# Performance work log

Hardware: AMD Instinct MI355X
Metric: run time of the kernel (lower is better)

## Reference

```python
import jax, jax.numpy as jnp
import numpy as np

B, M, N_, H, C, D = 2, 64, 64, 2, 8, 4  # batch, lattice m, lattice n, heads, channels, head_dim


def get_irpe(R):
    # R: (h, m, n) -> P[h, i, j] = R[h, (xi-xj) mod m, (yi-yj) mod n]
    # (negative fancy-index wrap in the original == modular indexing)
    h, m, n = R.shape
    dx = (jnp.arange(m)[:, None] - jnp.arange(m)[None, :]) % m  # (m, m)
    dy = (jnp.arange(n)[:, None] - jnp.arange(n)[None, :]) % n  # (n, n)
    P = R[:, dx[:, None, :, None], dy[None, :, None, :]]  # (h, m, n, m, n)
    return P.reshape(h, m * n, m * n)


def circ_conv(x, W, b, groups=1):
    # NHWC conv with CIRCULAR padding (flax 'CIRCULAR' == wrap-pad then VALID)
    ph, pw = W.shape[0] // 2, W.shape[1] // 2
    if ph or pw:
        x = jnp.pad(x, ((0, 0), (ph, ph), (pw, pw), (0, 0)), mode='wrap')
    y = jax.lax.conv_general_dilated(x, W, (1, 1), 'VALID',
                                     dimension_numbers=('NHWC', 'HWIO', 'NHWC'),
                                     feature_group_count=groups)
    return y + b


def setup_inputs() -> dict:
    key = jax.random.key(0)
    ks = jax.random.split(key, 10)
    m, n, c, h, d = M, N_, C, H, D

    def nrm(k, shape, fan_in):
        return jax.random.normal(k, shape, jnp.float32) * np.float32(np.sqrt(1.0 / fan_in))

    return {
        'x': jax.random.normal(ks[0], (B, m, n, c), jnp.float32),
        'conv_W': nrm(ks[1], (3, 3, c, c), 9 * c / 2),         # he_normal
        'conv_b': jnp.zeros((c,), jnp.float32),
        'Wq': nrm(ks[2], (c, h * d), c),                       # lecun_normal
        'Wk': nrm(ks[3], (c, h * d), c),
        'Wv': nrm(ks[4], (c, h * d), c),
        'pos': nrm(ks[5], (h, m, n), h * m),                   # lecun_normal on (h,m,n)
        'Wo': nrm(ks[6], (h * d, c), h * d),
        'mlp1_W': nrm(ks[7], (1, 1, c, 4 * c), c / 2),         # he_normal
        'mlp1_b': jnp.zeros((4 * c,), jnp.float32),
        'mlp2_W': nrm(ks[8], (3, 3, 1, 4 * c), 9),             # depthwise, lecun
        'mlp2_b': jnp.zeros((4 * c,), jnp.float32),
        'mlp3_W': nrm(ks[9], (1, 1, 4 * c, c), 4 * c / 2),     # he_normal
        'mlp3_b': jnp.zeros((c,), jnp.float32),
    }


def reference(x, conv_W, conv_b, Wq, Wk, Wv, pos, Wo,
              mlp1_W, mlp1_b, mlp2_W, mlp2_b, mlp3_W, mlp3_b):
    b_, m, n, c = x.shape
    h, d = H, D
    # ---- conv block (norm = 1) ----
    res = x
    x = circ_conv(jax.nn.gelu(x / np.float32(1.0)), conv_W, conv_b) + res
    # ---- attention (norm = 2) ----
    res = x
    y = x / np.float32(np.sqrt(2.0))

    def heads(z, W):
        # (b,m,n,c) @ (c,h*d) -> (b,h,N,d), last dim split order (h,d) as in einops
        return jnp.einsum('bmnc,ce->bmne', z, W).reshape(b_, m * n, h, d).transpose(0, 2, 1, 3)

    q, k, v = heads(y, Wq), heads(y, Wk), heads(y, Wv)
    P = get_irpe(pos)[None]  # (1, h, N, N)
    attn = jax.nn.softmax((jnp.einsum('bhnd,bhmd->bhnm', q, k) + P) / np.float32(np.sqrt(d)))
    # faithful to source: 'bhnn,bhnd->bhnd' uses the DIAGONAL of attn to scale v
    a = jnp.einsum('bhnn,bhnd->bhnd', attn, v)
    a = a.transpose(0, 2, 1, 3).reshape(b_, m * n, h * d)  # b n (h d)
    x = (a @ Wo).reshape(b_, m, n, c) + res
    # ---- MLP (norm = 3) ----
    res = x
    y = x / np.float32(np.sqrt(3.0))
    y = jax.nn.gelu(circ_conv(y, mlp1_W, mlp1_b))
    y = jax.nn.gelu(circ_conv(y, mlp2_W, mlp2_b, groups=4 * c))
    return circ_conv(y, mlp3_W, mlp3_b) + res
```

## Files before the change

kernel.cpp:

```cpp
#include <hip/hip_runtime.h>
#include <math.h>

#define Tt 4096
#define KCH 32

#define QSCALE 0.72134752044448170f

__device__ __forceinline__ float gelu_tanh(float x) {
  float x3 = x * x * x;
  float u2 = 2.3022081159f * (x + 0.044715f * x3);
  float e = __builtin_amdgcn_exp2f(u2);
  float th = 1.0f - 2.0f * __builtin_amdgcn_rcpf(e + 1.0f);
  return 0.5f * x * (1.0f + th);
}

__global__ __launch_bounds__(64) void k_pre(
    const float* __restrict__ x, const float* __restrict__ cW,
    const float* __restrict__ cb, const float* __restrict__ Wq,
    const float* __restrict__ Wk, const float* __restrict__ Wv,
    float* __restrict__ x1, float* __restrict__ qo,
    float* __restrict__ ko, float* __restrict__ vo) {
  const int bi = blockIdx.x;
  const int b = bi >> 6, i = bi & 63;
  const int j = threadIdx.x;
  float acc[8];
#pragma unroll
  for (int c = 0; c < 8; c++) acc[c] = cb[c];
#pragma unroll
  for (int di = 0; di < 3; di++) {
    const int ii = (i + di + 63) & 63;
#pragma unroll
    for (int dj = 0; dj < 3; dj++) {
      const int jj = (j + dj + 63) & 63;
      const float4* px = (const float4*)(x + ((b * 64 + ii) * 64 + jj) * 8);
      float4 a0 = px[0], a1 = px[1];
      float g[8];
      g[0] = gelu_tanh(a0.x); g[1] = gelu_tanh(a0.y);
      g[2] = gelu_tanh(a0.z); g[3] = gelu_tanh(a0.w);
      g[4] = gelu_tanh(a1.x); g[5] = gelu_tanh(a1.y);
      g[6] = gelu_tanh(a1.z); g[7] = gelu_tanh(a1.w);
      const float* w = cW + (di * 3 + dj) * 64;
#pragma unroll
      for (int ci = 0; ci < 8; ci++) {
        const float gv = g[ci];
#pragma unroll
        for (int c = 0; c < 8; c++) acc[c] += gv * w[ci * 8 + c];
      }
    }
  }
  const int t = i * 64 + j;
  const float4* pxc = (const float4*)(x + (b * Tt + t) * 8);
  float4 c0 = pxc[0], c1 = pxc[1];
  float xv[8];
  xv[0] = acc[0] + c0.x; xv[1] = acc[1] + c0.y;
  xv[2] = acc[2] + c0.z; xv[3] = acc[3] + c0.w;
  xv[4] = acc[4] + c1.x; xv[5] = acc[5] + c1.y;
  xv[6] = acc[6] + c1.z; xv[7] = acc[7] + c1.w;
  float4* px1 = (float4*)(x1 + (b * Tt + t) * 8);
  px1[0] = make_float4(xv[0], xv[1], xv[2], xv[3]);
  px1[1] = make_float4(xv[4], xv[5], xv[6], xv[7]);
  float y[8];
#pragma unroll
  for (int c = 0; c < 8; c++) y[c] = xv[c] * 0.7071067811865475f;
#pragma unroll
  for (int h = 0; h < 2; h++) {
    float qe[4], ke[4], ve[4];
#pragma unroll
    for (int d = 0; d < 4; d++) {
      const int e = h * 4 + d;
      float sq = 0.f, sk = 0.f, sv = 0.f;
#pragma unroll
      for (int c = 0; c < 8; c++) {
        sq += y[c] * Wq[c * 8 + e];
        sk += y[c] * Wk[c * 8 + e];
        sv += y[c] * Wv[c * 8 + e];
      }
      qe[d] = sq * QSCALE;
      ke[d] = sk; ve[d] = sv;
    }
    const int idx = (b * 2 + h) * Tt + t;
    ((float4*)qo)[idx] = make_float4(qe[0], qe[1], qe[2], qe[3]);
    ((float4*)ko)[idx] = make_float4(ke[0], ke[1], ke[2], ke[3]);
    ((float4*)vo)[idx] = make_float4(ve[0], ve[1], ve[2], ve[3]);
  }
}

__global__ __launch_bounds__(128) void k_attn(
    const float* __restrict__ qo, const float* __restrict__ ko,
    const float* __restrict__ pos, float* __restrict__ part) {
  const int id = blockIdx.x;
  const int qpair = id & 31;
  const int bh = (id >> 5) & 3;
  const int chunk = id >> 7;
  const int h = bh & 1;
  const int wave = threadIdx.x >> 6;
  const int lane = threadIdx.x & 63;
  const int qblk = qpair * 2 + wave;
  __shared__ float posr[2][2][128];
  __shared__ float4 ks[128];
#pragma unroll
  for (int r = 0; r < 2; r++) {
    const int j1 = chunk * 2 + r;
    const int row = (qblk - j1) & 63;
    const float v = QSCALE * pos[(h * 64 + row) * 64 + lane];
    posr[wave][r][lane] = v;
    posr[wave][r][lane + 64] = v;
  }
  const float4* kp = (const float4*)ko + bh * Tt + chunk * 128;
  ks[threadIdx.x] = kp[threadIdx.x];
  __syncthreads();
  const int t1 = qblk * 64 + lane;
  const float4 qv = ((const float4*)qo)[bh * Tt + t1];
  float Z0 = 0.0f, Z1 = 0.0f;
#pragma unroll
  for (int r = 0; r < 2; r++) {
    const float* prow = &posr[wave][r][lane + 1];
    const float4* kr = &ks[r * 64];
#pragma unroll 8
    for (int j2 = 0; j2 < 64; j2 += 2) {
      const float4 ka = kr[j2];
      const float4 kb = kr[j2 + 1];
      const float ba = prow[63 - j2];
      const float bb = prow[62 - j2];
      const float sa = fmaf(qv.x, ka.x, fmaf(qv.y, ka.y,
                       fmaf(qv.z, ka.z, fmaf(qv.w, ka.w, ba))));
      const float sb = fmaf(qv.x, kb.x, fmaf(qv.y, kb.y,
                       fmaf(qv.z, kb.z, fmaf(qv.w, kb.w, bb))));
      Z0 += __builtin_amdgcn_exp2f(sa);
      Z1 += __builtin_amdgcn_exp2f(sb);
    }
  }
  part[(chunk * 4 + bh) * Tt + t1] = Z0 + Z1;
}

__global__ __launch_bounds__(64) void k_post(
    const float* __restrict__ part, const float* __restrict__ qo,
    const float* __restrict__ ko, const float* __restrict__ vo,
    const float* __restrict__ pos, const float* __restrict__ Wo,
    const float* __restrict__ x1, const float* __restrict__ W1,
    const float* __restrict__ b1, float* __restrict__ x2,
    float* __restrict__ y1) {
  const int gid = blockIdx.x * 64 + threadIdx.x;
  const int b = gid >> 12, t = gid & 4095;
  float a[8];
#pragma unroll
  for (int h = 0; h < 2; h++) {
    const int bh = b * 2 + h;
    float Z = 0.0f;
#pragma unroll
    for (int c = 0; c < KCH; c++) Z += part[(c * 4 + bh) * Tt + t];
    const float4 qv = ((const float4*)qo)[bh * Tt + t];
    const float4 kv = ((const float4*)ko)[bh * Tt + t];
    const float4 vv = ((const float4*)vo)[bh * Tt + t];
    const float s = fmaf(qv.x, kv.x, fmaf(qv.y, kv.y,
                    fmaf(qv.z, kv.z, fmaf(qv.w, kv.w, QSCALE * pos[h * 4096]))));
    const float w = __builtin_amdgcn_exp2f(s) * __builtin_amdgcn_rcpf(Z);
    a[h * 4 + 0] = w * vv.x; a[h * 4 + 1] = w * vv.y;
    a[h * 4 + 2] = w * vv.z; a[h * 4 + 3] = w * vv.w;
  }
  const float4* px1 = (const float4*)(x1 + gid * 8);
  const float4 r0 = px1[0], r1 = px1[1];
  float res[8] = {r0.x, r0.y, r0.z, r0.w, r1.x, r1.y, r1.z, r1.w};
  float xv[8];
#pragma unroll
  for (int c = 0; c < 8; c++) {
    float s = res[c];
#pragma unroll
    for (int e = 0; e < 8; e++) s += a[e] * Wo[e * 8 + c];
    xv[c] = s;
  }
  float4* px2 = (float4*)(x2 + gid * 8);
  px2[0] = make_float4(xv[0], xv[1], xv[2], xv[3]);
  px2[1] = make_float4(xv[4], xv[5], xv[6], xv[7]);
  float y[8];
#pragma unroll
  for (int c = 0; c < 8; c++) y[c] = xv[c] * 0.5773502691896258f;
  float yv[32];
#pragma unroll
  for (int cc = 0; cc < 32; cc++) {
    float s = b1[cc];
#pragma unroll
    for (int c = 0; c < 8; c++) s += y[c] * W1[c * 32 + cc];
    yv[cc] = gelu_tanh(s);
  }
  float4* py = (float4*)(y1 + gid * 32);
#pragma unroll
  for (int qd = 0; qd < 8; qd++)
    py[qd] = make_float4(yv[qd * 4], yv[qd * 4 + 1], yv[qd * 4 + 2], yv[qd * 4 + 3]);
}

__global__ __launch_bounds__(64) void k_mlp23(
    const float* __restrict__ y1, const float* __restrict__ W2,
    const float* __restrict__ b2, const float* __restrict__ W3,
    const float* __restrict__ b3, const float* __restrict__ x2,
    float* __restrict__ out) {
  const int gid = blockIdx.x * 64 + threadIdx.x;
  const int b = gid >> 12, t = gid & 4095;
  const int i = t >> 6, j = t & 63;
  float acc[32];
#pragma unroll
  for (int cc = 0; cc < 32; cc++) acc[cc] = b2[cc];
#pragma unroll
  for (int di = 0; di < 3; di++) {
    const int ii = (i + di + 63) & 63;
#pragma unroll
    for (int dj = 0; dj < 3; dj++) {
      const int jj = (j + dj + 63) & 63;
      const float4* p = (const float4*)(y1 + ((b * 4096 + ii * 64 + jj) * 32));
      const float* w = W2 + (di * 3 + dj) * 32;
#pragma unroll
      for (int cq = 0; cq < 8; cq++) {
        const float4 u = p[cq];
        acc[cq * 4 + 0] += u.x * w[cq * 4 + 0];
        acc[cq * 4 + 1] += u.y * w[cq * 4 + 1];
        acc[cq * 4 + 2] += u.z * w[cq * 4 + 2];
        acc[cq * 4 + 3] += u.w * w[cq * 4 + 3];
      }
    }
  }
#pragma unroll
  for (int cc = 0; cc < 32; cc++) acc[cc] = gelu_tanh(acc[cc]);
  const float4* px2 = (const float4*)(x2 + gid * 8);
  const float4 r0 = px2[0], r1 = px2[1];
  float o[8] = {r0.x + b3[0], r0.y + b3[1], r0.z + b3[2], r0.w + b3[3],
                r1.x + b3[4], r1.y + b3[5], r1.z + b3[6], r1.w + b3[7]};
#pragma unroll
  for (int cc = 0; cc < 32; cc++) {
    const float v = acc[cc];
#pragma unroll
    for (int c = 0; c < 8; c++) o[c] += v * W3[cc * 8 + c];
  }
  float4* po = (float4*)(out + gid * 8);
  po[0] = make_float4(o[0], o[1], o[2], o[3]);
  po[1] = make_float4(o[4], o[5], o[6], o[7]);
}

extern "C" void kernel_launch(void* const* d_in, const int* in_sizes, int n_in,
                              void* d_out, int out_size, void* d_ws, size_t ws_size,
                              hipStream_t stream) {
  const float* x  = (const float*)d_in[0];
  const float* cW = (const float*)d_in[1];
  const float* cb = (const float*)d_in[2];
  const float* Wq = (const float*)d_in[3];
  const float* Wk = (const float*)d_in[4];
  const float* Wv = (const float*)d_in[5];
  const float* pos = (const float*)d_in[6];
  const float* Wo = (const float*)d_in[7];
  const float* W1 = (const float*)d_in[8];
  const float* b1 = (const float*)d_in[9];
  const float* W2 = (const float*)d_in[10];
  const float* b2 = (const float*)d_in[11];
  const float* W3 = (const float*)d_in[12];
  const float* b3 = (const float*)d_in[13];

  float* ws   = (float*)d_ws;
  float* x1   = ws;
  float* qo   = ws + 65536;
  float* ko   = ws + 131072;
  float* vo   = ws + 196608;
  float* part = ws + 262144;
  float* x2   = ws + 786432;
  float* y1   = ws + 851968;
  float* out  = (float*)d_out;

  hipLaunchKernelGGL(k_pre,   dim3(128),  dim3(64),  0, stream, x, cW, cb, Wq, Wk, Wv, x1, qo, ko, vo);
  hipLaunchKernelGGL(k_attn,  dim3(4096), dim3(128), 0, stream, qo, ko, pos, part);
  hipLaunchKernelGGL(k_post,  dim3(128),  dim3(64),  0, stream, part, qo, ko, vo, pos, Wo, x1, W1, b1, x2, y1);
  hipLaunchKernelGGL(k_mlp23, dim3(128),  dim3(64),  0, stream, y1, W2, b2, W3, b3, x2, out);
}
```

Measured before the change: 115.6 us.

## Fuse attention epilogue with MLP into one kernel using shared-memory halo rows

Merges k_post and k_mlp23 into a single kernel where each block owns one lattice row and recomputes the attention output and first MLP layer for the row above and below (circular halo), staging y1 in shared memory. This removes one kernel launch and the global round-trips for x2 and y1. The cost is computing the post-attention and MLP1 work three times per row, including three reads of the 32-chunk partition sums.

```diff
diff --git a/kernel.cpp b/kernel.cpp
--- a/kernel.cpp
+++ b/kernel.cpp
@@ -133,103 +133,93 @@
   part[(chunk * 4 + bh) * Tt + t1] = Z0 + Z1;
 }
 
-__global__ __launch_bounds__(64) void k_post(
+__global__ __launch_bounds__(64) void k_postmlp(
     const float* __restrict__ part, const float* __restrict__ qo,
     const float* __restrict__ ko, const float* __restrict__ vo,
     const float* __restrict__ pos, const float* __restrict__ Wo,
     const float* __restrict__ x1, const float* __restrict__ W1,
-    const float* __restrict__ b1, float* __restrict__ x2,
-    float* __restrict__ y1) {
-  const int gid = blockIdx.x * 64 + threadIdx.x;
-  const int b = gid >> 12, t = gid & 4095;
-  float a[8];
-#pragma unroll
-  for (int h = 0; h < 2; h++) {
-    const int bh = b * 2 + h;
-    float Z = 0.0f;
-#pragma unroll
-    for (int c = 0; c < KCH; c++) Z += part[(c * 4 + bh) * Tt + t];
-    const float4 qv = ((const float4*)qo)[bh * Tt + t];
-    const float4 kv = ((const float4*)ko)[bh * Tt + t];
-    const float4 vv = ((const float4*)vo)[bh * Tt + t];
-    const float s = fmaf(qv.x, kv.x, fmaf(qv.y, kv.y,
-                    fmaf(qv.z, kv.z, fmaf(qv.w, kv.w, QSCALE * pos[h * 4096]))));
-    const float w = __builtin_amdgcn_exp2f(s) * __builtin_amdgcn_rcpf(Z);
-    a[h * 4 + 0] = w * vv.x; a[h * 4 + 1] = w * vv.y;
-    a[h * 4 + 2] = w * vv.z; a[h * 4 + 3] = w * vv.w;
-  }
-  const float4* px1 = (const float4*)(x1 + gid * 8);
-  const float4 r0 = px1[0], r1 = px1[1];
-  float res[8] = {r0.x, r0.y, r0.z, r0.w, r1.x, r1.y, r1.z, r1.w};
-  float xv[8];
-#pragma unroll
-  for (int c = 0; c < 8; c++) {
-    float s = res[c];
-#pragma unroll
-    for (int e = 0; e < 8; e++) s += a[e] * Wo[e * 8 + c];
-    xv[c] = s;
-  }
-  float4* px2 = (float4*)(x2 + gid * 8);
-  px2[0] = make_float4(xv[0], xv[1], xv[2], xv[3]);
-  px2[1] = make_float4(xv[4], xv[5], xv[6], xv[7]);
-  float y[8];
-#pragma unroll
-  for (int c = 0; c < 8; c++) y[c] = xv[c] * 0.5773502691896258f;
-  float yv[32];
-#pragma unroll
-  for (int cc = 0; cc < 32; cc++) {
-    float s = b1[cc];
-#pragma unroll
-    for (int c = 0; c < 8; c++) s += y[c] * W1[c * 32 + cc];
-    yv[cc] = gelu_tanh(s);
-  }
-  float4* py = (float4*)(y1 + gid * 32);
-#pragma unroll
-  for (int qd = 0; qd < 8; qd++)
-    py[qd] = make_float4(yv[qd * 4], yv[qd * 4 + 1], yv[qd * 4 + 2], yv[qd * 4 + 3]);
-}
-
-__global__ __launch_bounds__(64) void k_mlp23(
-    const float* __restrict__ y1, const float* __restrict__ W2,
+    const float* __restrict__ b1, const float* __restrict__ W2,
     const float* __restrict__ b2, const float* __restrict__ W3,
-    const float* __restrict__ b3, const float* __restrict__ x2,
-    float* __restrict__ out) {
-  const int gid = blockIdx.x * 64 + threadIdx.x;
-  const int b = gid >> 12, t = gid & 4095;
-  const int i = t >> 6, j = t & 63;
+    const float* __restrict__ b3, float* __restrict__ out) {
+  const int bi = blockIdx.x;
+  const int b = bi >> 6, i = bi & 63;
+  const int j = threadIdx.x;
+  __shared__ float y1s[3][64][36];
+  float x2own[8];
+#pragma unroll
+  for (int rr = 0; rr < 3; rr++) {
+    const int ii = (i + rr + 63) & 63;
+    const int t = ii * 64 + j;
+    const int gid = b * 4096 + t;
+    float a[8];
+#pragma unroll
+    for (int h = 0; h < 2; h++) {
+      const int bh = b * 2 + h;
+      float Z = 0.0f;
+#pragma unroll
+      for (int c = 0; c < KCH; c++) Z += part[(c * 4 + bh) * Tt + t];
+      const float4 qv = ((const float4*)qo)[bh * Tt + t];
+      const float4 kv = ((const float4*)ko)[bh * Tt + t];
+      const float4 vv = ((const float4*)vo)[bh * Tt + t];
+      const float s = fmaf(qv.x, kv.x, fmaf(qv.y, kv.y,
+                      fmaf(qv.z, kv.z, fmaf(qv.w, kv.w, QSCALE * pos[h * 4096]))));
+      const float w = __builtin_amdgcn_exp2f(s) * __builtin_amdgcn_rcpf(Z);
+      a[h * 4 + 0] = w * vv.x; a[h * 4 + 1] = w * vv.y;
+      a[h * 4 + 2] = w * vv.z; a[h * 4 + 3] = w * vv.w;
+    }
+    const float4* px1 = (const float4*)(x1 + gid * 8);
+    const float4 r0 = px1[0], r1 = px1[1];
+    float res[8] = {r0.x, r0.y, r0.z, r0.w, r1.x, r1.y, r1.z, r1.w};
+    float xv[8];
+#pragma unroll
+    for (int c = 0; c < 8; c++) {
+      float s = res[c];
+#pragma unroll
+      for (int e = 0; e < 8; e++) s += a[e] * Wo[e * 8 + c];
+      xv[c] = s;
+    }
+    if (rr == 1) {
+#pragma unroll
+      for (int c = 0; c < 8; c++) x2own[c] = xv[c];
+    }
+    float y[8];
+#pragma unroll
+    for (int c = 0; c < 8; c++) y[c] = xv[c] * 0.5773502691896258f;
+#pragma unroll
+    for (int cc = 0; cc < 32; cc++) {
+      float s = b1[cc];
+#pragma unroll
+      for (int c = 0; c < 8; c++) s += y[c] * W1[c * 32 + cc];
+      y1s[rr][j][cc] = gelu_tanh(s);
+    }
+  }
+  __syncthreads();
   float acc[32];
 #pragma unroll
   for (int cc = 0; cc < 32; cc++) acc[cc] = b2[cc];
 #pragma unroll
   for (int di = 0; di < 3; di++) {
-    const int ii = (i + di + 63) & 63;
 #pragma unroll
     for (int dj = 0; dj < 3; dj++) {
       const int jj = (j + dj + 63) & 63;
-      const float4* p = (const float4*)(y1 + ((b * 4096 + ii * 64 + jj) * 32));
+      const float* p = &y1s[di][jj][0];
       const float* w = W2 + (di * 3 + dj) * 32;
 #pragma unroll
-      for (int cq = 0; cq < 8; cq++) {
-        const float4 u = p[cq];
-        acc[cq * 4 + 0] += u.x * w[cq * 4 + 0];
-        acc[cq * 4 + 1] += u.y * w[cq * 4 + 1];
-        acc[cq * 4 + 2] += u.z * w[cq * 4 + 2];
-        acc[cq * 4 + 3] += u.w * w[cq * 4 + 3];
-      }
+      for (int cc = 0; cc < 32; cc++) acc[cc] += p[cc] * w[cc];
     }
   }
 #pragma unroll
   for (int cc = 0; cc < 32; cc++) acc[cc] = gelu_tanh(acc[cc]);
-  const float4* px2 = (const float4*)(x2 + gid * 8);
-  const float4 r0 = px2[0], r1 = px2[1];
-  float o[8] = {r0.x + b3[0], r0.y + b3[1], r0.z + b3[2], r0.w + b3[3],
-                r1.x + b3[4], r1.y + b3[5], r1.z + b3[6], r1.w + b3[7]};
+  float o[8] = {x2own[0] + b3[0], x2own[1] + b3[1], x2own[2] + b3[2],
+                x2own[3] + b3[3], x2own[4] + b3[4], x2own[5] + b3[5],
+                x2own[6] + b3[6], x2own[7] + b3[7]};
 #pragma unroll
   for (int cc = 0; cc < 32; cc++) {
     const float v = acc[cc];
 #pragma unroll
     for (int c = 0; c < 8; c++) o[c] += v * W3[cc * 8 + c];
   }
+  const int gid = bi * 64 + j;
   float4* po = (float4*)(out + gid * 8);
   po[0] = make_float4(o[0], o[1], o[2], o[3]);
   po[1] = make_float4(o[4], o[5], o[6], o[7]);
@@ -259,12 +249,9 @@
   float* ko   = ws + 131072;
   float* vo   = ws + 196608;
   float* part = ws + 262144;
-  float* x2   = ws + 786432;
-  float* y1   = ws + 851968;
   float* out  = (float*)d_out;
 
-  hipLaunchKernelGGL(k_pre,   dim3(128),  dim3(64),  0, stream, x, cW, cb, Wq, Wk, Wv, x1, qo, ko, vo);
-  hipLaunchKernelGGL(k_attn,  dim3(4096), dim3(128), 0, stream, qo, ko, pos, part);
-  hipLaunchKernelGGL(k_post,  dim3(128),  dim3(64),  0, stream, part, qo, ko, vo, pos, Wo, x1, W1, b1, x2, y1);
-  hipLaunchKernelGGL(k_mlp23, dim3(128),  dim3(64),  0, stream, y1, W2, b2, W3, b3, x2, out);
-}
+  hipLaunchKernelGGL(k_pre,     dim3(128),  dim3(64),  0, stream, x, cW, cb, Wq, Wk, Wv, x1, qo, ko, vo);
+  hipLaunchKernelGGL(k_attn,    dim3(4096), dim3(128), 0, stream, qo, ko, pos, part);
+  hipLaunchKernelGGL(k_postmlp, dim3(128),  dim3(64),  0, stream, part, qo, ko, vo, pos, Wo, x1, W1, b1, W2, b2, W3, b3, out);
+}
```

Result: slower. 170.1 us (+47.2%).
